# Kernel optimization log

Hardware: AMD Instinct MI355X
Metric: run time of the kernel (lower is better)

The kernel has to match this reference:

```python
import jax, jax.numpy as jnp
import numpy as np

H = 4096       # hidden_size
NH = 32        # num attention heads
DN = 128       # qk_nope_head_dim
DR = 64        # qk_rope_head_dim
DV = 128       # v_head_dim
QL = 1536      # q_lora_rank
KL = 512       # kv_lora_rank
INH = 32       # indexer heads
IHD = 128      # indexer head_dim (== fp8 quant block -> one scale per head)
TOPK = 512     # index_topk
T = 1024       # prefill tokens
SCALING = (DN + DR) ** -0.5
FP8_MAX = 448.0  # e4m3 max


def _rms(x, w, eps=1e-6):
    return x * jax.lax.rsqrt(jnp.mean(x * x, -1, keepdims=True) + eps) * w


def _ln(x, w, b, eps=1e-6):
    m = jnp.mean(x, -1, keepdims=True)
    v = jnp.mean(jnp.square(x - m), -1, keepdims=True)
    return (x - m) * jax.lax.rsqrt(v + eps) * w + b


def _rope(x, pos):
    # interleaved (non-neox) rotary embedding on the last dim
    d = x.shape[-1]
    inv = 1.0 / (10000.0 ** (jnp.arange(0, d, 2, dtype=jnp.float32) / d))
    ang = pos.astype(jnp.float32)[:, None] * inv  # [T, d/2]
    shape = (x.shape[0],) + (1,) * (x.ndim - 2) + (d // 2,)
    cos = jnp.cos(ang).reshape(shape)
    sin = jnp.sin(ang).reshape(shape)
    x1, x2 = x[..., 0::2], x[..., 1::2]
    return jnp.stack([x1 * cos - x2 * sin, x1 * sin + x2 * cos], -1).reshape(x.shape)


def _forward(hidden_states, w_qkv_a, q_a_ln_w, w_q_b, kv_a_ln_w, w_kv_b, w_o,
             w_idx_qb, w_idx_k, idx_k_ln_w, idx_k_ln_b, w_idx_weights, positions):
    Tq = hidden_states.shape[0]
    neg = jnp.finfo(jnp.float32).min
    # --- fused low-rank QKV-a projection ---
    qkv_a = hidden_states @ w_qkv_a                       # [T, QL+KL+DR]
    q_c, kv_c, k_pe = qkv_a[:, :QL], qkv_a[:, QL:QL + KL], qkv_a[:, QL + KL:]
    q_cn = _rms(q_c, q_a_ln_w)                            # qr (normed q latent)
    # --- MLA decompression ---
    q = (q_cn @ w_q_b).reshape(Tq, NH, DN + DR)
    q_nope, q_pe = q[..., :DN], q[..., DN:]
    kv = (_rms(kv_c, kv_a_ln_w) @ w_kv_b).reshape(Tq, NH, DN + DV)
    k_nope, v = kv[..., :DN], kv[..., DN:]
    q_pe = _rope(q_pe, positions)
    k_pe = _rope(k_pe, positions)                         # [T, DR], shared across heads (MQA)
    # --- lightning indexer (fp8 ue8m0 per-token-group quant emulated in fp32) ---
    qi = (q_cn @ w_idx_qb).reshape(Tq, INH, IHD)
    qi = jnp.concatenate([_rope(qi[..., :DR], positions), qi[..., DR:]], -1)
    ki = _ln(hidden_states @ w_idx_k, idx_k_ln_w, idx_k_ln_b)   # [T, IHD]
    ki = jnp.concatenate([_rope(ki[:, :DR], positions), ki[:, DR:]], -1)
    amax = jnp.max(jnp.abs(qi), -1, keepdims=True)        # group == head (IHD == block 128)
    q_scale = jnp.exp2(jnp.ceil(jnp.log2(jnp.maximum(amax, 1e-10) / FP8_MAX)))  # ue8m0
    qi_q = qi / q_scale                                   # values in fp8 range
    wts = (hidden_states @ w_idx_weights) * q_scale[..., 0]
    wts = wts * (IHD ** -0.5) * (INH ** -0.5)             # [T, INH]
    sim = jax.nn.relu(jnp.einsum('qhd,kd->hqk', qi_q, ki))
    logits = jnp.einsum('qh,hqk->qk', wts, sim)           # [Tq, Tk]
    idx = jnp.arange(Tq)
    causal = idx[:, None] >= idx[None, :]
    logits = jnp.where(causal, logits, neg)
    _, topk_idx = jax.lax.top_k(logits, TOPK)             # [T, TOPK]
    sparse_mask = jnp.zeros((Tq, Tq), bool).at[idx[:, None], topk_idx].set(True) & causal
    # --- sparse MLA attention ---
    qf = jnp.concatenate([q_nope, q_pe], -1)              # [T, NH, DN+DR]
    kf = jnp.concatenate([k_nope, jnp.broadcast_to(k_pe[:, None, :], (Tq, NH, DR))], -1)
    scores = jnp.einsum('qhd,khd->hqk', qf, kf) * SCALING
    scores = jnp.where(sparse_mask[None], scores, neg)
    attn = jax.nn.softmax(scores, -1)
    out = jnp.einsum('hqk,khd->qhd', attn, v).reshape(Tq, NH * DV)
    return out @ w_o                                      # [T, H]


def setup_inputs() -> dict:
    key = jax.random.key(0)
    ks = jax.random.split(key, 8)
    s = 0.02
    return {
        'hidden_states': jax.random.normal(ks[0], (T, H), jnp.float32),
        'positions': jnp.arange(T, dtype=jnp.int32),
        'w_qkv_a': jax.random.normal(ks[1], (H, QL + KL + DR), jnp.float32) * s,
        'q_a_ln_w': jnp.ones((QL,), jnp.float32),
        'w_q_b': jax.random.normal(ks[2], (QL, NH * (DN + DR)), jnp.float32) * s,
        'kv_a_ln_w': jnp.ones((KL,), jnp.float32),
        'w_kv_b': jax.random.normal(ks[3], (KL, NH * (DN + DV)), jnp.float32) * s,
        'w_o': jax.random.normal(ks[4], (NH * DV, H), jnp.float32) * s,
        'w_idx_qb': jax.random.normal(ks[5], (QL, INH * IHD), jnp.float32) * s,
        'w_idx_k': jax.random.normal(ks[6], (H, IHD), jnp.float32) * s,
        'idx_k_ln_w': jnp.ones((IHD,), jnp.float32),
        'idx_k_ln_b': jnp.zeros((IHD,), jnp.float32),
        'w_idx_weights': jax.random.normal(ks[7], (H, INH), jnp.float32) * s,
    }


def reference(hidden_states, positions, w_qkv_a, q_a_ln_w, w_q_b, kv_a_ln_w, w_kv_b, w_o,
              w_idx_qb, w_idx_k, idx_k_ln_w, idx_k_ln_b, w_idx_weights):
    return _forward(hidden_states, w_qkv_a, q_a_ln_w, w_q_b, kv_a_ln_w, w_kv_b, w_o,
                    w_idx_qb, w_idx_k, idx_k_ln_w, idx_k_ln_b, w_idx_weights, positions)
```

## Files before the change

kernel.cpp:

```cpp
#include <hip/hip_runtime.h>
#include <hip/hip_bf16.h>
#include <math.h>
#include <type_traits>

#define TT   1024
#define HH   4096
#define NHH  32
#define DNN  128
#define DRR  64
#define DVV  128
#define QLL  1536
#define KLL  512
#define INHH 32
#define IHDD 128
#define TOPKK 512
#define SKS  16
#define SKC  (HH / SKS)
#define QKVN 2112

typedef __attribute__((ext_vector_type(8))) short short8;
typedef __attribute__((ext_vector_type(4))) short short4v;
typedef __attribute__((ext_vector_type(4))) float f32x4;

static __device__ __constant__ float kScaling = 0.07216878364870322f;
static __device__ __constant__ float kWtsScale = 0.015625f;

static __device__ __forceinline__ short f2bf(float f) {
  unsigned u = __float_as_uint(f);
  unsigned r = (u + 0x7fffu + ((u >> 16) & 1u)) >> 16;
  return (short)r;
}
static __device__ __forceinline__ float bf2f(short s) {
  return __uint_as_float(((unsigned)(unsigned short)s) << 16);
}
static __device__ __forceinline__ void gl16(const void* g, void* l) {
  __builtin_amdgcn_global_load_lds(
      (const __attribute__((address_space(1))) unsigned int*)g,
      (__attribute__((address_space(3))) unsigned int*)l, 16, 0, 0);
}
static __device__ __forceinline__ int xcd_swz(int n, int nwg) {
  const int q = nwg >> 3, r = nwg & 7;
  const int x = n & 7, i = n >> 3;
  return (x < r ? x * (q + 1) : r * (q + 1) + (x - r) * q) + i;
}

__global__ __launch_bounds__(256) void skinny_splitk(const float* __restrict__ A,
                                                     const float* __restrict__ B1,
                                                     const float* __restrict__ B2,
                                                     float* __restrict__ part) {
  __shared__ float As[8][64];
  __shared__ float Bs[8][160];
  const int tid = threadIdx.x;
  const int tx = tid & 15, ty = tid >> 4;
  const int bm = blockIdx.x * 64;
  const int kbase = blockIdx.y * SKC;
  float acc[4][10];
#pragma unroll
  for (int i = 0; i < 4; ++i)
#pragma unroll
    for (int j = 0; j < 10; ++j) acc[i][j] = 0.f;
  const int am = tid >> 1, aj = (tid & 1) * 4;
  for (int k0 = 0; k0 < SKC; k0 += 8) {
    __syncthreads();
    if (tid < 128) {
      float4 av = *(const float4*)(A + (size_t)(bm + am) * HH + kbase + k0 + aj);
      As[aj + 0][am] = av.x; As[aj + 1][am] = av.y;
      As[aj + 2][am] = av.z; As[aj + 3][am] = av.w;
    }
#pragma unroll
    for (int i = 0; i < 2; ++i) {
      const int idx = tid + i * 256;
      if (idx < 320) {
        const int row = idx / 40;
        const int c = (idx - row * 40) * 4;
        float4 bv;
        if (c < 128) bv = *(const float4*)(B1 + (size_t)(kbase + k0 + row) * 128 + c);
        else         bv = *(const float4*)(B2 + (size_t)(kbase + k0 + row) * 32 + (c - 128));
        *(float4*)&Bs[row][c] = bv;
      }
    }
    __syncthreads();
#pragma unroll
    for (int p = 0; p < 8; ++p) {
      float av[4];
#pragma unroll
      for (int i = 0; i < 4; ++i) av[i] = As[p][ty * 4 + i];
      float bv[10];
#pragma unroll
      for (int j = 0; j < 10; ++j) bv[j] = Bs[p][tx * 10 + j];
#pragma unroll
      for (int i = 0; i < 4; ++i)
#pragma unroll
        for (int j = 0; j < 10; ++j) acc[i][j] = fmaf(av[i], bv[j], acc[i][j]);
    }
  }
  float* dst = part + ((size_t)blockIdx.y * TT + bm) * 160;
#pragma unroll
  for (int i = 0; i < 4; ++i)
#pragma unroll
    for (int j = 0; j < 10; ++j)
      dst[(size_t)(ty * 4 + i) * 160 + tx * 10 + j] = acc[i][j];
}

__global__ __launch_bounds__(256) void skinny_reduce(const float* __restrict__ part,
                                                     float* __restrict__ kib,
                                                     float* __restrict__ wtsb) {
  const int idx = blockIdx.x * 256 + threadIdx.x;
  const int m = idx / 160, c = idx - m * 160;
  float s = 0.f;
#pragma unroll
  for (int ks = 0; ks < SKS; ++ks) s += part[((size_t)ks * TT + m) * 160 + c];
  if (c < 128) kib[(size_t)m * 128 + c] = s;
  else wtsb[(size_t)m * 32 + (c - 128)] = s;
}

template <typename CT>
__global__ __launch_bounds__(256) void gemm_bf16(const short* __restrict__ A,
                                                 const short* __restrict__ Bt,
                                                 CT* __restrict__ C,
                                                 int M, int N, int K) {
  __shared__ short As[64 * 64];
  __shared__ short Bs[128 * 64];
  int flat = blockIdx.x + gridDim.x * blockIdx.y;
  flat = xcd_swz(flat, gridDim.x * gridDim.y);
  const int byg = flat % gridDim.y;
  const int bxg = flat / gridDim.y;
  const int tid = threadIdx.x;
  const int lane = tid & 63, wv = tid >> 6;
  const int wc = wv * 32;
  const int bm = byg * 64, bn = bxg * 128;
  const int l15 = lane & 15, l4 = lane >> 4;
  const int sx = (l15 & 7) * 8;
  f32x4 acc[4][2];
#pragma unroll
  for (int i = 0; i < 4; ++i)
#pragma unroll
    for (int j = 0; j < 2; ++j) acc[i][j] = f32x4{0.f, 0.f, 0.f, 0.f};
  for (int k0 = 0; k0 < K; k0 += 64) {
    __syncthreads();
#pragma unroll
    for (int i = 0; i < 2; ++i) {
      const int idx = tid + i * 256;
      const int row = idx >> 3, c8 = (idx & 7) * 8;
      const int cs = c8 ^ ((row & 7) * 8);
      gl16(A + (size_t)(bm + row) * K + k0 + cs, &As[idx * 8]);
    }
#pragma unroll
    for (int i = 0; i < 4; ++i) {
      const int idx = tid + i * 256;
      const int row = idx >> 3, c8 = (idx & 7) * 8;
      const int cs = c8 ^ ((row & 7) * 8);
      gl16(Bt + (size_t)(bn + row) * K + k0 + cs, &Bs[idx * 8]);
    }
    __syncthreads();
    short8 fa[4][2], fb[2][2];
#pragma unroll
    for (int rt = 0; rt < 4; ++rt)
#pragma unroll
      for (int kk = 0; kk < 2; ++kk)
        fa[rt][kk] = *(const short8*)(&As[(rt * 16 + l15) * 64 + ((kk * 32 + l4 * 8) ^ sx)]);
#pragma unroll
    for (int ct = 0; ct < 2; ++ct)
#pragma unroll
      for (int kk = 0; kk < 2; ++kk)
        fb[ct][kk] = *(const short8*)(&Bs[(wc + ct * 16 + l15) * 64 + ((kk * 32 + l4 * 8) ^ sx)]);
#pragma unroll
    for (int kk = 0; kk < 2; ++kk)
#pragma unroll
      for (int rt = 0; rt < 4; ++rt)
#pragma unroll
        for (int ct = 0; ct < 2; ++ct)
          acc[rt][ct] = __builtin_amdgcn_mfma_f32_16x16x32_bf16(fa[rt][kk], fb[ct][kk], acc[rt][ct], 0, 0, 0);
  }
#pragma unroll
  for (int rt = 0; rt < 4; ++rt)
#pragma unroll
    for (int ct = 0; ct < 2; ++ct)
#pragma unroll
      for (int r = 0; r < 4; ++r) {
        const int row = bm + rt * 16 + l4 * 4 + r;
        const int col = bn + wc + ct * 16 + l15;
        const float v = acc[rt][ct][r];
        if constexpr (std::is_same<CT, float>::value) C[(size_t)row * N + col] = v;
        else C[(size_t)row * N + col] = __float2bfloat16(v);
      }
}

__global__ __launch_bounds__(256) void gemm1_splitk(const short* __restrict__ A,
                                                    const short* __restrict__ Bt,
                                                    float* __restrict__ part,
                                                    int M, int Np, int K, int kchunk) {
  __shared__ short As[64 * 64];
  __shared__ short Bs[128 * 64];
  int flat = blockIdx.x + gridDim.x * (blockIdx.y + gridDim.y * blockIdx.z);
  flat = xcd_swz(flat, gridDim.x * gridDim.y * gridDim.z);
  const int byg = flat % gridDim.y;
  int tmp = flat / gridDim.y;
  const int bxg = tmp % gridDim.x, bzg = tmp / gridDim.x;
  const int tid = threadIdx.x;
  const int lane = tid & 63, wv = tid >> 6;
  const int wc = wv * 32;
  const int bm = byg * 64, bn = bxg * 128;
  const int kbeg = bzg * kchunk;
  const int l15 = lane & 15, l4 = lane >> 4;
  const int sx = (l15 & 7) * 8;
  f32x4 acc[4][2];
#pragma unroll
  for (int i = 0; i < 4; ++i)
#pragma unroll
    for (int j = 0; j < 2; ++j) acc[i][j] = f32x4{0.f, 0.f, 0.f, 0.f};
  for (int k0 = kbeg; k0 < kbeg + kchunk; k0 += 64) {
    __syncthreads();
#pragma unroll
    for (int i = 0; i < 2; ++i) {
      const int idx = tid + i * 256;
      const int row = idx >> 3, c8 = (idx & 7) * 8;
      const int cs = c8 ^ ((row & 7) * 8);
      gl16(A + (size_t)(bm + row) * K + k0 + cs, &As[idx * 8]);
    }
#pragma unroll
    for (int i = 0; i < 4; ++i) {
      const int idx = tid + i * 256;
      const int row = idx >> 3, c8 = (idx & 7) * 8;
      const int cs = c8 ^ ((row & 7) * 8);
      gl16(Bt + (size_t)(bn + row) * K + k0 + cs, &Bs[idx * 8]);
    }
    __syncthreads();
    short8 fa[4][2], fb[2][2];
#pragma unroll
    for (int rt = 0; rt < 4; ++rt)
#pragma unroll
      for (int kk = 0; kk < 2; ++kk)
        fa[rt][kk] = *(const short8*)(&As[(rt * 16 + l15) * 64 + ((kk * 32 + l4 * 8) ^ sx)]);
#pragma unroll
    for (int ct = 0; ct < 2; ++ct)
#pragma unroll
      for (int kk = 0; kk < 2; ++kk)
        fb[ct][kk] = *(const short8*)(&Bs[(wc + ct * 16 + l15) * 64 + ((kk * 32 + l4 * 8) ^ sx)]);
#pragma unroll
    for (int kk = 0; kk < 2; ++kk)
#pragma unroll
      for (int rt = 0; rt < 4; ++rt)
#pragma unroll
        for (int ct = 0; ct < 2; ++ct)
          acc[rt][ct] = __builtin_amdgcn_mfma_f32_16x16x32_bf16(fa[rt][kk], fb[ct][kk], acc[rt][ct], 0, 0, 0);
  }
  float* dst = part + (size_t)bzg * M * Np;
#pragma unroll
  for (int rt = 0; rt < 4; ++rt)
#pragma unroll
    for (int ct = 0; ct < 2; ++ct)
#pragma unroll
      for (int r = 0; r < 4; ++r)
        dst[(size_t)(bm + rt * 16 + l4 * 4 + r) * Np + bn + wc + ct * 16 + l15] =
            acc[rt][ct][r];
}

__global__ __launch_bounds__(256) void gemm3(const short* __restrict__ Ah,
                                             const short* __restrict__ Al,
                                             const short* __restrict__ Bth,
                                             const short* __restrict__ Btl,
                                             float* __restrict__ part,
                                             int M, int Np, int K, int kchunk) {
  __shared__ short AS[64 * 64], BS[128 * 64];
  int flat = blockIdx.x + gridDim.x * (blockIdx.y + gridDim.y * blockIdx.z);
  flat = xcd_swz(flat, gridDim.x * gridDim.y * gridDim.z);
  const int byg = flat % gridDim.y;
  int tmp = flat / gridDim.y;
  const int bxg = tmp % gridDim.x, bzg = tmp / gridDim.x;
  const int tid = threadIdx.x;
  const int lane = tid & 63, wv = tid >> 6;
  const int wc = wv * 32;
  const int l15 = lane & 15, l4 = lane >> 4;
  const int sx = (l15 & 7) * 8;
  const int bm = byg * 64, bn = bxg * 128;
  const int kbeg = bzg * kchunk;
  f32x4 acc[4][2];
#pragma unroll
  for (int i = 0; i < 4; ++i)
#pragma unroll
    for (int j = 0; j < 2; ++j) acc[i][j] = f32x4{0.f, 0.f, 0.f, 0.f};
  for (int k0 = kbeg; k0 < kbeg + kchunk; k0 += 32) {
    __syncthreads();
#pragma unroll
    for (int i = 0; i < 2; ++i) {
      const int idx = tid + i * 256;
      const int row = idx >> 3, c8 = (idx & 7) * 8;
      const int cs = c8 ^ ((row & 7) * 8);
      const short* srcA = (cs < 32) ? (Ah + (size_t)(bm + row) * K + k0 + cs)
                                    : (Al + (size_t)(bm + row) * K + k0 + (cs - 32));
      gl16(srcA, &AS[idx * 8]);
    }
#pragma unroll
    for (int i = 0; i < 4; ++i) {
      const int idx = tid + i * 256;
      const int row = idx >> 3, c8 = (idx & 7) * 8;
      const int cs = c8 ^ ((row & 7) * 8);
      const short* srcB = (cs < 32) ? (Bth + (size_t)(bn + row) * K + k0 + cs)
                                    : (Btl + (size_t)(bn + row) * K + k0 + (cs - 32));
      gl16(srcB, &BS[idx * 8]);
    }
    __syncthreads();
    short8 fah[4], fal[4], fbh[2], fbl[2];
#pragma unroll
    for (int rt = 0; rt < 4; ++rt) {
      const int row = rt * 16 + l15;
      fah[rt] = *(const short8*)&AS[row * 64 + ((l4 * 8) ^ sx)];
      fal[rt] = *(const short8*)&AS[row * 64 + ((32 + l4 * 8) ^ sx)];
    }
#pragma unroll
    for (int ct = 0; ct < 2; ++ct) {
      const int row = wc + ct * 16 + l15;
      fbh[ct] = *(const short8*)&BS[row * 64 + ((l4 * 8) ^ sx)];
      fbl[ct] = *(const short8*)&BS[row * 64 + ((32 + l4 * 8) ^ sx)];
    }
#pragma unroll
    for (int ct = 0; ct < 2; ++ct)
#pragma unroll
      for (int rt = 0; rt < 4; ++rt) {
        acc[rt][ct] = __builtin_amdgcn_mfma_f32_16x16x32_bf16(fah[rt], fbh[ct], acc[rt][ct], 0, 0, 0);
        acc[rt][ct] = __builtin_amdgcn_mfma_f32_16x16x32_bf16(fah[rt], fbl[ct], acc[rt][ct], 0, 0, 0);
        acc[rt][ct] = __builtin_amdgcn_mfma_f32_16x16x32_bf16(fal[rt], fbh[ct], acc[rt][ct], 0, 0, 0);
      }
  }
  float* dst = part + (size_t)bzg * M * Np;
#pragma unroll
  for (int rt = 0; rt < 4; ++rt)
#pragma unroll
    for (int ct = 0; ct < 2; ++ct)
#pragma unroll
      for (int r = 0; r < 4; ++r)
        dst[(size_t)(bm + rt * 16 + l4 * 4 + r) * Np + bn + wc + ct * 16 + l15] =
            acc[rt][ct][r];
}

__global__ __launch_bounds__(256) void reduce_splitk(const float* __restrict__ part,
                                                     float* __restrict__ C,
                                                     int M, int Np, int Nout, int ldC,
                                                     int ksplit) {
  const int c = blockIdx.x * 256 + threadIdx.x;
  const int m = blockIdx.y;
  if (c >= Nout) return;
  float s = 0.f;
  for (int z = 0; z < ksplit; ++z) s += part[((size_t)z * M + m) * Np + c];
  C[(size_t)m * ldC + c] = s;
}

__global__ __launch_bounds__(256) void qkv_post(const float* __restrict__ qpart,
                                                const float* __restrict__ tpart,
                                                const float* __restrict__ q_ln_w,
                                                const float* __restrict__ kv_ln_w,
                                                const int* __restrict__ pos,
                                                short* __restrict__ qcn_bf,
                                                short* __restrict__ qcn_lo,
                                                short* __restrict__ kvn_bf,
                                                short* __restrict__ kpe_bf) {
  const int t = blockIdx.x, tid = threadIdx.x;
  __shared__ float red[4];
  float qv[6];
  float ss = 0.f;
#pragma unroll
  for (int j = 0; j < 6; ++j) {
    const int c = tid + j * 256;
    float s = 0.f;
#pragma unroll
    for (int z = 0; z < 4; ++z) s += qpart[((size_t)z * TT + t) * QLL + c];
    qv[j] = s;
    ss = fmaf(s, s, ss);
  }
#pragma unroll
  for (int o = 32; o > 0; o >>= 1) ss += __shfl_xor(ss, o);
  if ((tid & 63) == 0) red[tid >> 6] = ss;
  __syncthreads();
  const float rq = rsqrtf((red[0] + red[1] + red[2] + red[3]) / (float)QLL + 1e-6f);
  __syncthreads();
#pragma unroll
  for (int j = 0; j < 6; ++j) {
    const int c = tid + j * 256;
    const float v = qv[j] * rq * q_ln_w[c];
    const short h = f2bf(v);
    qcn_bf[(size_t)t * QLL + c] = h;
    qcn_lo[(size_t)t * QLL + c] = f2bf(v - bf2f(h));
  }
  float kv2[2];
  float ss2 = 0.f;
#pragma unroll
  for (int j = 0; j < 2; ++j) {
    const int c = tid + j * 256;
    float s = 0.f;
#pragma unroll
    for (int z = 0; z < 4; ++z) s += tpart[((size_t)z * TT + t) * 640 + c];
    kv2[j] = s;
    ss2 = fmaf(s, s, ss2);
  }
#pragma unroll
  for (int o = 32; o > 0; o >>= 1) ss2 += __shfl_xor(ss2, o);
  if ((tid & 63) == 0) red[tid >> 6] = ss2;
  __syncthreads();
  const float rkv = rsqrtf((red[0] + red[1] + red[2] + red[3]) / (float)KLL + 1e-6f);
#pragma unroll
  for (int j = 0; j < 2; ++j) {
    const int c = tid + j * 256;
    kvn_bf[(size_t)t * KLL + c] = f2bf(kv2[j] * rkv * kv_ln_w[c]);
  }
  if (tid < 32) {
    float x1 = 0.f, x2 = 0.f;
#pragma unroll
    for (int z = 0; z < 4; ++z) {
      x1 += tpart[((size_t)z * TT + t) * 640 + 512 + 2 * tid];
      x2 += tpart[((size_t)z * TT + t) * 640 + 512 + 2 * tid + 1];
    }
    const float inv = powf(10000.f, -(float)tid * (1.f / 32.f));
    float sn, cs;
    sincosf((float)pos[t] * inv, &sn, &cs);
    kpe_bf[(size_t)t * 64 + 2 * tid]     = f2bf(x1 * cs - x2 * sn);
    kpe_bf[(size_t)t * 64 + 2 * tid + 1] = f2bf(x1 * sn + x2 * cs);
  }
}

__global__ __launch_bounds__(256) void split_cast(const float* __restrict__ in,
                                                  short* __restrict__ hi,
                                                  short* __restrict__ lo, int n4) {
  const int i = blockIdx.x * 256 + threadIdx.x;
  if (i >= n4) return;
  float4 v = *(const float4*)(in + (size_t)i * 4);
  float av[4] = {v.x, v.y, v.z, v.w};
  short4v h, l;
#pragma unroll
  for (int e = 0; e < 4; ++e) {
    h[e] = f2bf(av[e]);
    l[e] = f2bf(av[e] - bf2f(h[e]));
  }
  *(short4v*)(hi + (size_t)i * 4) = h;
  *(short4v*)(lo + (size_t)i * 4) = l;
}

__global__ __launch_bounds__(256) void transpose_cast_g(const float* __restrict__ B,
                                                        short* __restrict__ Bt,
                                                        int K, int ldB, int col0, int Ncols) {
  __shared__ float tile[64][65];
  const int tid = threadIdx.x;
  const int k0 = blockIdx.y * 64, n0 = blockIdx.x * 64;
  const int nl = tid >> 3, kc = (tid & 7) * 8;
  if (n0 >= Ncols) {
    short8 z = {0, 0, 0, 0, 0, 0, 0, 0};
#pragma unroll
    for (int i = 0; i < 2; ++i) {
      const int n = nl + i * 32;
      *(short8*)(Bt + (size_t)(n0 + n) * K + k0 + kc) = z;
    }
    return;
  }
  const int r = tid >> 4, c4 = (tid & 15) * 4;
#pragma unroll
  for (int i = 0; i < 4; ++i) {
    float4 v = *(const float4*)(B + (size_t)(k0 + r + i * 16) * ldB + col0 + n0 + c4);
    tile[r + i * 16][c4 + 0] = v.x;
    tile[r + i * 16][c4 + 1] = v.y;
    tile[r + i * 16][c4 + 2] = v.z;
    tile[r + i * 16][c4 + 3] = v.w;
  }
  __syncthreads();
#pragma unroll
  for (int i = 0; i < 2; ++i) {
    const int n = nl + i * 32;
    short8 o;
#pragma unroll
    for (int e = 0; e < 8; ++e) o[e] = f2bf(tile[kc + e][n]);
    *(short8*)(Bt + (size_t)(n0 + n) * K + k0 + kc) = o;
  }
}

__global__ __launch_bounds__(256) void transpose_split_cast(const float* __restrict__ B,
                                                            short* __restrict__ Bth,
                                                            short* __restrict__ Btl,
                                                            int K, int ldB, int col0,
                                                            int Ncols) {
  __shared__ float tile[64][65];
  const int tid = threadIdx.x;
  const int k0 = blockIdx.y * 64, n0 = blockIdx.x * 64;
  const int nl = tid >> 3, kc = (tid & 7) * 8;
  if (n0 >= Ncols) {
    short8 z = {0, 0, 0, 0, 0, 0, 0, 0};
#pragma unroll
    for (int i = 0; i < 2; ++i) {
      const int n = nl + i * 32;
      *(short8*)(Bth + (size_t)(n0 + n) * K + k0 + kc) = z;
      *(short8*)(Btl + (size_t)(n0 + n) * K + k0 + kc) = z;
    }
    return;
  }
  const int r = tid >> 4, c4 = (tid & 15) * 4;
#pragma unroll
  for (int i = 0; i < 4; ++i) {
    float4 v = *(const float4*)(B + (size_t)(k0 + r + i * 16) * ldB + col0 + n0 + c4);
    tile[r + i * 16][c4 + 0] = v.x;
    tile[r + i * 16][c4 + 1] = v.y;
    tile[r + i * 16][c4 + 2] = v.z;
    tile[r + i * 16][c4 + 3] = v.w;
  }
  __syncthreads();
#pragma unroll
  for (int i = 0; i < 2; ++i) {
    const int n = nl + i * 32;
    short8 oh, ol;
#pragma unroll
    for (int e = 0; e < 8; ++e) {
      const float x = tile[kc + e][n];
      oh[e] = f2bf(x);
      ol[e] = f2bf(x - bf2f(oh[e]));
    }
    *(short8*)(Bth + (size_t)(n0 + n) * K + k0 + kc) = oh;
    *(short8*)(Btl + (size_t)(n0 + n) * K + k0 + kc) = ol;
  }
}

__global__ __launch_bounds__(128) void ki_prep(const float* __restrict__ kin,
                                               const float* __restrict__ w,
                                               const float* __restrict__ b,
                                               const int* __restrict__ pos,
                                               short* __restrict__ kih,
                                               short* __restrict__ kil) {
  const int t = blockIdx.x, i = threadIdx.x;
  float v = kin[(size_t)t * 128 + i];
  float s = v;
#pragma unroll
  for (int o = 32; o > 0; o >>= 1) s += __shfl_xor(s, o);
  __shared__ float r1[2], r2[2];
  if ((i & 63) == 0) r1[i >> 6] = s;
  __syncthreads();
  const float m = (r1[0] + r1[1]) * (1.f / 128.f);
  const float dv = v - m;
  float sq = dv * dv;
#pragma unroll
  for (int o = 32; o > 0; o >>= 1) sq += __shfl_xor(sq, o);
  if ((i & 63) == 0) r2[i >> 6] = sq;
  __syncthreads();
  const float var = (r2[0] + r2[1]) * (1.f / 128.f);
  float x = dv * rsqrtf(var + 1e-6f) * w[i] + b[i];
  if (i < 64) {
    const float part = __shfl_xor(x, 1);
    const int pi = i >> 1;
    const float inv = powf(10000.f, -(float)pi * (1.f / 32.f));
    float sn, cs;
    sincosf((float)pos[t] * inv, &sn, &cs);
    x = (i & 1) ? (part * sn + x * cs) : (x * cs - part * sn);
  }
  const short h = f2bf(x);
  kih[(size_t)t * 128 + i] = h;
  kil[(size_t)t * 128 + i] = f2bf(x - bf2f(h));
}

__global__ void q_rope_repack(const short* __restrict__ qbuf,
                              short* __restrict__ qhout,
                              const int* __restrict__ pos) {
  const int q = blockIdx.x, h = blockIdx.y;
  const int p = threadIdx.x;
  const short* s = qbuf + ((size_t)q * 32 + h) * 192;
  short* d = qhout + ((size_t)h * 1024 + q) * 192;
  float x1 = bf2f(s[2 * p]), x2 = bf2f(s[2 * p + 1]);
  if (p >= 64) {
    const int i = p - 64;
    const float inv = powf(10000.f, -(float)i * (1.f / 32.f));
    const float ang = (float)pos[q] * inv;
    float sn, cs;
    sincosf(ang, &sn, &cs);
    const float a = x1 * cs - x2 * sn, b = x1 * sn + x2 * cs;
    x1 = a; x2 = b;
  }
  d[2 * p]     = f2bf(x1);
  d[2 * p + 1] = f2bf(x2);
}

__global__ __launch_bounds__(256) void qi_rope_repack_split(const float* __restrict__ qib,
                                                            const int* __restrict__ pos,
                                                            short* __restrict__ qhh,
                                                            short* __restrict__ qhl) {
  const int qt = blockIdx.x, h = blockIdx.y;
  const int tid = threadIdx.x;
#pragma unroll
  for (int i = 0; i < 8; ++i) {
    const int idx = tid + i * 256;
    const int q = idx >> 5, c = idx & 31;
    float4 v = *(const float4*)(qib + ((size_t)(qt * 64 + q) * 32 + h) * 128 + c * 4);
    float av[4] = {v.x, v.y, v.z, v.w};
    if (c < 16) {
      const int qg = qt * 64 + q;
      const float p = (float)pos[qg];
      float sn0, cs0, sn1, cs1;
      sincosf(p * powf(10000.f, -(float)(c * 2) * (1.f / 32.f)), &sn0, &cs0);
      sincosf(p * powf(10000.f, -(float)(c * 2 + 1) * (1.f / 32.f)), &sn1, &cs1);
      const float a0 = av[0] * cs0 - av[1] * sn0, a1 = av[0] * sn0 + av[1] * cs0;
      const float a2 = av[2] * cs1 - av[3] * sn1, a3 = av[2] * sn1 + av[3] * cs1;
      av[0] = a0; av[1] = a1; av[2] = a2; av[3] = a3;
    }
    short4v hv, lv;
#pragma unroll
    for (int e = 0; e < 4; ++e) {
      hv[e] = f2bf(av[e]);
      lv[e] = f2bf(av[e] - bf2f(hv[e]));
    }
    const size_t off = ((size_t)h * 1024 + qt * 64 + q) * 128 + c * 4;
    *(short4v*)(qhh + off) = hv;
    *(short4v*)(qhl + off) = lv;
  }
}

__global__ __launch_bounds__(256) void kv_repack(const short* __restrict__ kvb,
                                                 const short* __restrict__ kpe,
                                                 short* __restrict__ kfout,
                                                 short* __restrict__ vtout) {
  const int kt = blockIdx.x, h = blockIdx.y;
  const int tid = threadIdx.x;
  const int k0 = kt * 64;
  __shared__ short vtile[64][136];
#pragma unroll
  for (int i = 0; i < 6; ++i) {
    const int idx = tid + i * 256;
    const int row = idx / 24, c = idx - row * 24;
    short8 v = (c < 16) ? *(const short8*)(kvb + ((size_t)(k0 + row) * 32 + h) * 256 + c * 8)
                        : *(const short8*)(kpe + (size_t)(k0 + row) * 64 + (c - 16) * 8);
    *(short8*)(kfout + ((size_t)h * 1024 + k0 + row) * 192 + c * 8) = v;
  }
#pragma unroll
  for (int i = 0; i < 4; ++i) {
    const int idx = tid + i * 256;
    const int row = idx >> 4, c = idx & 15;
    *(short8*)&vtile[row][c * 8] =
        *(const short8*)(kvb + ((size_t)(k0 + row) * 32 + h) * 256 + 128 + c * 8);
  }
  __syncthreads();
#pragma unroll
  for (int i = 0; i < 4; ++i) {
    const int idx = tid + i * 256;
    const int d = idx >> 3, kc = idx & 7;
    short8 o;
#pragma unroll
    for (int e = 0; e < 8; ++e) o[e] = vtile[kc * 8 + e][d];
    *(short8*)(vtout + ((size_t)h * 128 + d) * 1024 + k0 + kc * 8) = o;
  }
}

__global__ __launch_bounds__(256) void logits_mfma(const short* __restrict__ qih,
                                                   const short* __restrict__ qil,
                                                   const short* __restrict__ kih_g,
                                                   const short* __restrict__ kil_g,
                                                   const float* __restrict__ wts,
                                                   float* __restrict__ part) {
  const int bid = blockIdx.x;
  int bq = (int)((sqrtf(8.f * bid + 1.f) - 1.f) * 0.5f);
  while ((bq + 1) * (bq + 2) / 2 <= bid) ++bq;
  while (bq * (bq + 1) / 2 > bid) --bq;
  const int bk = bid - bq * (bq + 1) / 2;
  const int g = blockIdx.y;
  __shared__ short kih[64 * 128], kil[64 * 128];
  __shared__ float swts[64][16];
  const int tid = threadIdx.x;
  const int lane = tid & 63, wv = tid >> 6;
  const int wr = (wv >> 1) * 32, wc = (wv & 1) * 32;
  const int l15 = lane & 15, l4 = lane >> 4;
  const int q0 = bq * 64, k0 = bk * 64;
  {
    const int r0 = tid >> 4;
    const int c8 = (tid & 15) * 8;
#pragma unroll
    for (int i = 0; i < 4; ++i) {
      const int row = r0 + i * 16;
      gl16(kih_g + (size_t)(k0 + row) * 128 + c8, &kih[(tid + i * 256) * 8]);
      gl16(kil_g + (size_t)(k0 + row) * 128 + c8, &kil[(tid + i * 256) * 8]);
    }
  }
#pragma unroll
  for (int i = 0; i < 4; ++i) {
    const int idx = tid + i * 256;
    swts[idx >> 4][idx & 15] = wts[(size_t)(q0 + (idx >> 4)) * 32 + g * 16 + (idx & 15)];
  }
  __syncthreads();
  short8 kbh[2][4], kbl[2][4];
#pragma unroll
  for (int ct = 0; ct < 2; ++ct)
#pragma unroll
    for (int ks = 0; ks < 4; ++ks) {
      kbh[ct][ks] = *(const short8*)&kih[(wc + ct * 16 + l15) * 128 + ks * 32 + l4 * 8];
      kbl[ct][ks] = *(const short8*)&kil[(wc + ct * 16 + l15) * 128 + ks * 32 + l4 * 8];
    }
  f32x4 lacc[2][2];
#pragma unroll
  for (int i = 0; i < 2; ++i)
#pragma unroll
    for (int j = 0; j < 2; ++j) lacc[i][j] = f32x4{0.f, 0.f, 0.f, 0.f};
  for (int hh = 0; hh < 16; ++hh) {
    const int h = g * 16 + hh;
    short8 qah[2][4], qal[2][4];
#pragma unroll
    for (int rt = 0; rt < 2; ++rt)
#pragma unroll
      for (int ks = 0; ks < 4; ++ks) {
        const size_t off = ((size_t)h * 1024 + q0 + wr + rt * 16 + l15) * 128 + ks * 32 + l4 * 8;
        qah[rt][ks] = *(const short8*)(qih + off);
        qal[rt][ks] = *(const short8*)(qil + off);
      }
    f32x4 hacc[2][2];
#pragma unroll
    for (int i = 0; i < 2; ++i)
#pragma unroll
      for (int j = 0; j < 2; ++j) hacc[i][j] = f32x4{0.f, 0.f, 0.f, 0.f};
#pragma unroll
    for (int ks = 0; ks < 4; ++ks)
#pragma unroll
      for (int rt = 0; rt < 2; ++rt)
#pragma unroll
        for (int ct = 0; ct < 2; ++ct) {
          hacc[rt][ct] = __builtin_amdgcn_mfma_f32_16x16x32_bf16(qah[rt][ks], kbh[ct][ks], hacc[rt][ct], 0, 0, 0);
          hacc[rt][ct] = __builtin_amdgcn_mfma_f32_16x16x32_bf16(qah[rt][ks], kbl[ct][ks], hacc[rt][ct], 0, 0, 0);
          hacc[rt][ct] = __builtin_amdgcn_mfma_f32_16x16x32_bf16(qal[rt][ks], kbh[ct][ks], hacc[rt][ct], 0, 0, 0);
        }
#pragma unroll
    for (int rt = 0; rt < 2; ++rt)
#pragma unroll
      for (int ct = 0; ct < 2; ++ct)
#pragma unroll
        for (int r = 0; r < 4; ++r) {
          const int row = wr + rt * 16 + l4 * 4 + r;
          const float w = swts[row][hh] * kWtsScale;
          lacc[rt][ct][r] = fmaf(w, fmaxf(hacc[rt][ct][r], 0.f), lacc[rt][ct][r]);
        }
  }
#pragma unroll
  for (int rt = 0; rt < 2; ++rt)
#pragma unroll
    for (int ct = 0; ct < 2; ++ct)
#pragma unroll
      for (int r = 0; r < 4; ++r)
        part[(size_t)g * TT * TT + (size_t)(q0 + wr + rt * 16 + l4 * 4 + r) * TT +
             (k0 + wc + ct * 16 + l15)] = lacc[rt][ct][r];
}

__global__ __launch_bounds__(256) void topk_mask(const float* __restrict__ part,
                                                 unsigned* __restrict__ maskbuf) {
  const int w = threadIdx.x >> 6;
  const int lane = threadIdx.x & 63;
  const int q = blockIdx.x * 4 + w;
  const size_t NN = (size_t)TT * TT;
  __shared__ unsigned long long bl[4][16];
  unsigned v[16];
#pragma unroll
  for (int j = 0; j < 16; ++j) {
    const int k = j * 64 + lane;
    unsigned uv = 0u;
    if (k <= q) {
      const size_t o = (size_t)q * TT + k;
      const float s = part[o] + part[NN + o];
      unsigned bb = __float_as_uint(s);
      uv = (bb & 0x80000000u) ? ~bb : (bb | 0x80000000u);
    }
    v[j] = uv;
  }
  if (q + 1 <= TOPKK) {
#pragma unroll
    for (int j = 0; j < 16; ++j) {
      const unsigned long long m = __ballot(j * 64 + lane <= q);
      if (lane == 0) bl[w][j] = m;
    }
  } else {
    unsigned lo = 1u, hi = 0xFFFFFFFFu;
    while (lo < hi) {
      const unsigned mid = lo + ((hi - lo) >> 1) + ((hi - lo) & 1u);
      int c = 0;
#pragma unroll
      for (int j = 0; j < 16; ++j) c += __popcll(__ballot(v[j] >= mid));
      if (c >= TOPKK) lo = mid; else hi = mid - 1u;
    }
    const unsigned ustar = lo;
    int nGreater = 0;
#pragma unroll
    for (int j = 0; j < 16; ++j) nGreater += __popcll(__ballot(v[j] > ustar));
    int need = TOPKK - nGreater;
    const unsigned long long lanemask = lane ? (~0ull >> (64 - lane)) : 0ull;
#pragma unroll
    for (int j = 0; j < 16; ++j) {
      const unsigned long long bg = __ballot(v[j] > ustar);
      const unsigned long long be = __ballot(v[j] == ustar);
      const int ce = __popcll(be);
      const int take = need < ce ? need : ce;
      const int rank = __popcll(be & lanemask);
      const bool selme = ((be >> lane) & 1ull) && (rank < take);
      const unsigned long long m = bg | __ballot(selme);
      if (lane == 0) bl[w][j] = m;
      need -= take;
    }
  }
  __builtin_amdgcn_s_waitcnt(0);
  if (lane < 32)
    maskbuf[(size_t)q * 32 + lane] = (unsigned)(bl[w][lane >> 1] >> ((lane & 1) * 32));
}

__global__ __launch_bounds__(256) void attn_mfma(const short* __restrict__ qh,
                                                 const short* __restrict__ kf,
                                                 const short* __restrict__ vt,
                                                 const unsigned* __restrict__ maskbuf,
                                                 short* __restrict__ ao) {
  const int h = blockIdx.x;
  const int yy = blockIdx.y;
  const int qt = (yy < 8) ? (yy * 2) : (31 - yy * 2);
  const int tid = threadIdx.x;
  const int lane = tid & 63, w = tid >> 6;
  const int l15 = lane & 15, l4 = lane >> 4;
  const int q0 = qt * 64;
  __shared__ short kfs[64 * 200];
  __shared__ short vts[128 * 72];
  __shared__ short ps[4][16][72];
  __shared__ unsigned m32s[64][2];
  short8 qf[6];
#pragma unroll
  for (int ks = 0; ks < 6; ++ks)
    qf[ks] = *(const short8*)(qh + ((size_t)h * 1024 + q0 + w * 16 + l15) * 192 + ks * 32 + l4 * 8);
  f32x4 of[8];
#pragma unroll
  for (int dt = 0; dt < 8; ++dt) of[dt] = f32x4{0.f, 0.f, 0.f, 0.f};
  float m[4], l[4];
#pragma unroll
  for (int r = 0; r < 4; ++r) { m[r] = -INFINITY; l[r] = 0.f; }

  for (int kt = 0; kt <= qt; ++kt) {
    const int k0 = kt * 64;
    __syncthreads();
#pragma unroll
    for (int i = 0; i < 6; ++i) {
      const int idx = tid + i * 256;
      const int row = idx / 24, c = idx - row * 24;
      *(short8*)&kfs[row * 200 + c * 8] =
          *(const short8*)(kf + ((size_t)h * 1024 + k0 + row) * 192 + c * 8);
    }
#pragma unroll
    for (int i = 0; i < 4; ++i) {
      const int idx = tid + i * 256;
      const int row = idx >> 3, c = idx & 7;
      *(short8*)&vts[row * 72 + c * 8] =
          *(const short8*)(vt + ((size_t)h * 128 + row) * 1024 + k0 + c * 8);
    }
    if (tid < 128)
      m32s[tid >> 1][tid & 1] = maskbuf[(size_t)(q0 + (tid >> 1)) * 32 + (k0 >> 5) + (tid & 1)];
    __syncthreads();
    f32x4 sacc[4];
#pragma unroll
    for (int j = 0; j < 4; ++j) sacc[j] = f32x4{0.f, 0.f, 0.f, 0.f};
#pragma unroll
    for (int ks = 0; ks < 6; ++ks)
#pragma unroll
      for (int j = 0; j < 4; ++j) {
        short8 kb = *(const short8*)&kfs[(j * 16 + l15) * 200 + ks * 32 + l4 * 8];
        sacc[j] = __builtin_amdgcn_mfma_f32_16x16x32_bf16(qf[ks], kb, sacc[j], 0, 0, 0);
      }
    float tmax[4] = {-INFINITY, -INFINITY, -INFINITY, -INFINITY};
#pragma unroll
    for (int j = 0; j < 4; ++j)
#pragma unroll
      for (int r = 0; r < 4; ++r) {
        const int kcol = j * 16 + l15;
        const unsigned um = m32s[w * 16 + l4 * 4 + r][kcol >> 5];
        float s = sacc[j][r] * kScaling;
        s = ((um >> (kcol & 31)) & 1u) ? s : -INFINITY;
        sacc[j][r] = s;
        tmax[r] = fmaxf(tmax[r], s);
      }
#pragma unroll
    for (int r = 0; r < 4; ++r) {
      tmax[r] = fmaxf(tmax[r], __shfl_xor(tmax[r], 1));
      tmax[r] = fmaxf(tmax[r], __shfl_xor(tmax[r], 2));
      tmax[r] = fmaxf(tmax[r], __shfl_xor(tmax[r], 4));
      tmax[r] = fmaxf(tmax[r], __shfl_xor(tmax[r], 8));
    }
    float f[4];
#pragma unroll
    for (int r = 0; r < 4; ++r) {
      const float mn = fmaxf(m[r], tmax[r]);
      f[r] = __expf(fmaxf(m[r], -1e30f) - fmaxf(mn, -1e30f));
      m[r] = mn;
      l[r] *= f[r];
    }
    float psum[4] = {0.f, 0.f, 0.f, 0.f};
#pragma unroll
    for (int j = 0; j < 4; ++j)
#pragma unroll
      for (int r = 0; r < 4; ++r) {
        const float p = __expf(sacc[j][r] - fmaxf(m[r], -1e30f));
        psum[r] += p;
        ps[w][l4 * 4 + r][j * 16 + l15] = f2bf(p);
      }
#pragma unroll
    for (int r = 0; r < 4; ++r) {
      psum[r] += __shfl_xor(psum[r], 1);
      psum[r] += __shfl_xor(psum[r], 2);
      psum[r] += __shfl_xor(psum[r], 4);
      psum[r] += __shfl_xor(psum[r], 8);
      l[r] += psum[r];
    }
#pragma unroll
    for (int dt = 0; dt < 8; ++dt)
#pragma unroll
      for (int r = 0; r < 4; ++r) of[dt][r] *= f[r];
    short8 pa0 = *(const short8*)&ps[w][l15][l4 * 8];
    short8 pa1 = *(const short8*)&ps[w][l15][32 + l4 * 8];
#pragma unroll
    for (int dt = 0; dt < 8; ++dt) {
      short8 vb0 = *(const short8*)&vts[(dt * 16 + l15) * 72 + l4 * 8];
      short8 vb1 = *(const short8*)&vts[(dt * 16 + l15) * 72 + 32 + l4 * 8];
      of[dt] = __builtin_amdgcn_mfma_f32_16x16x32_bf16(pa0, vb0, of[dt], 0, 0, 0);
      of[dt] = __builtin_amdgcn_mfma_f32_16x16x32_bf16(pa1, vb1, of[dt], 0, 0, 0);
    }
  }
#pragma unroll
  for (int r = 0; r < 4; ++r) {
    const float invl = 1.f / l[r];
#pragma unroll
    for (int dt = 0; dt < 8; ++dt)
      ao[(size_t)(q0 + w * 16 + l4 * 4 + r) * 4096 + h * 128 + dt * 16 + l15] =
          f2bf(of[dt][r] * invl);
  }
}

extern "C" void kernel_launch(void* const* d_in, const int* in_sizes, int n_in,
                              void* d_out, int out_size, void* d_ws, size_t ws_size,
                              hipStream_t stream) {
  const float* hidden     = (const float*)d_in[0];
  const int*   positions  = (const int*)d_in[1];
  const float* w_qkv_a    = (const float*)d_in[2];
  const float* q_a_ln_w   = (const float*)d_in[3];
  const float* w_q_b      = (const float*)d_in[4];
  const float* kv_a_ln_w  = (const float*)d_in[5];
  const float* w_kv_b     = (const float*)d_in[6];
  const float* w_o        = (const float*)d_in[7];
  const float* w_idx_qb   = (const float*)d_in[8];
  const float* w_idx_k    = (const float*)d_in[9];
  const float* idx_k_ln_w = (const float*)d_in[10];
  const float* idx_k_ln_b = (const float*)d_in[11];
  const float* w_idx_w    = (const float*)d_in[12];
  float* out = (float*)d_out;

  float* ws = (float*)d_ws;
  size_t off = 0;
  auto take = [&](size_t n) { float* p = ws + off; off += n; return p; };
  short* qcn_bf  = (short*)take((size_t)TT * QLL / 2);
  short* qcn_lo  = (short*)take((size_t)TT * QLL / 2);
  short* kvn_bf  = (short*)take((size_t)TT * KLL / 2);
  short* qbuf    = (short*)take((size_t)TT * NHH * 192 / 2);
  short* kvbuf   = (short*)take((size_t)TT * NHH * 256 / 2);
  short* kpe_bf  = (short*)take((size_t)TT * 32);
  float* qib     = take((size_t)TT * INHH * IHDD);
  float* kib     = take((size_t)TT * IHDD);
  float* wtsb    = take((size_t)TT * INHH);
  short* kih_g   = (short*)take((size_t)TT * IHDD / 2);
  short* kil_g   = (short*)take((size_t)TT * IHDD / 2);
  short* qhb     = (short*)take((size_t)NHH * TT * 192 / 2);
  short* qih_h   = (short*)take((size_t)INHH * TT * 128 / 2);
  short* qih_l   = (short*)take((size_t)INHH * TT * 128 / 2);
  short* kfb     = (short*)take((size_t)NHH * TT * 192 / 2);
  short* vtb     = (short*)take((size_t)NHH * 128 * TT / 2);
  float* part4   = take((size_t)4 * TT * TT);
  unsigned* maskbuf = (unsigned*)take((size_t)TT * 32);
  short* hid_h   = (short*)take((size_t)TT * HH / 2);
  short* hid_l   = (short*)take((size_t)TT * HH / 2);
  short* wqkva_h = (short*)take((size_t)QLL * HH / 2);
  short* wqkva_l = (short*)take((size_t)QLL * HH / 2);
  short* wtail_t = (short*)take((size_t)640 * HH / 2);
  short* widxqb_h = (short*)take((size_t)HH * QLL / 2);
  short* widxqb_l = (short*)take((size_t)HH * QLL / 2);
  short* wqb_t   = (short*)take((size_t)6144 * QLL / 2);
  short* wkvb_t  = (short*)take((size_t)8192 * KLL / 2);
  short* ao   = (short*)part4;
  short* wo_t = hid_h;
  float* skpart = part4;
  float* qkvpart = (float*)vtb;
  float* tailpart = (float*)kvbuf;
  float* idxpart = (float*)qhb;

  const dim3 blk(256);
  skinny_splitk<<<dim3(16, SKS), blk, 0, stream>>>(hidden, w_idx_k, w_idx_w, skpart);
  skinny_reduce<<<dim3(TT * 160 / 256), blk, 0, stream>>>(skpart, kib, wtsb);
  split_cast<<<dim3(TT * HH / 4 / 256), blk, 0, stream>>>(hidden, hid_h, hid_l, TT * HH / 4);
  transpose_split_cast<<<dim3(QLL / 64, HH / 64), blk, 0, stream>>>(w_qkv_a, wqkva_h, wqkva_l, HH, QKVN, 0, QLL);
  transpose_cast_g<<<dim3(640 / 64, HH / 64), blk, 0, stream>>>(w_qkv_a, wtail_t, HH, QKVN, QLL, QKVN - QLL);
  transpose_split_cast<<<dim3(HH / 64, QLL / 64), blk, 0, stream>>>(w_idx_qb, widxqb_h, widxqb_l, QLL, HH, 0, HH);
  transpose_cast_g<<<dim3(6144 / 64, QLL / 64), blk, 0, stream>>>(w_q_b, wqb_t, QLL, 6144, 0, 6144);
  transpose_cast_g<<<dim3(8192 / 64, KLL / 64), blk, 0, stream>>>(w_kv_b, wkvb_t, KLL, 8192, 0, 8192);
  ki_prep<<<TT, 128, 0, stream>>>(kib, idx_k_ln_w, idx_k_ln_b, positions, kih_g, kil_g);
  gemm3<<<dim3(QLL / 128, 16, 4), blk, 0, stream>>>(hid_h, hid_l, wqkva_h, wqkva_l,
                                                    qkvpart, TT, QLL, HH, HH / 4);
  gemm1_splitk<<<dim3(5, 16, 4), blk, 0, stream>>>(hid_h, wtail_t, tailpart, TT, 640, HH, HH / 4);
  qkv_post<<<dim3(TT), blk, 0, stream>>>(qkvpart, tailpart, q_a_ln_w, kv_a_ln_w, positions,
                                         qcn_bf, qcn_lo, kvn_bf, kpe_bf);
  transpose_cast_g<<<dim3(HH / 64, HH / 64), blk, 0, stream>>>(w_o, wo_t, HH, HH, 0, HH);
  gemm3<<<dim3(HH / 128, 16, 2), blk, 0, stream>>>(qcn_bf, qcn_lo, widxqb_h, widxqb_l,
                                                   idxpart, TT, HH, QLL, QLL / 2);
  reduce_splitk<<<dim3(HH / 256, TT), blk, 0, stream>>>(idxpart, qib, TT, HH, HH, HH, 2);
  gemm_bf16<__hip_bfloat16><<<dim3(48, 16), blk, 0, stream>>>(qcn_bf, wqb_t, (__hip_bfloat16*)qbuf, TT, 6144, QLL);
  gemm_bf16<__hip_bfloat16><<<dim3(64, 16), blk, 0, stream>>>(kvn_bf, wkvb_t, (__hip_bfloat16*)kvbuf, TT, 8192, KLL);
  q_rope_repack<<<dim3(TT, NHH), 96, 0, stream>>>(qbuf, qhb, positions);
  qi_rope_repack_split<<<dim3(16, INHH), blk, 0, stream>>>(qib, positions, qih_h, qih_l);
  kv_repack<<<dim3(16, NHH), blk, 0, stream>>>(kvbuf, kpe_bf, kfb, vtb);
  logits_mfma<<<dim3(136, 2), blk, 0, stream>>>(qih_h, qih_l, kih_g, kil_g, wtsb, part4);
  topk_mask<<<dim3(TT / 4), blk, 0, stream>>>(part4, maskbuf);
  attn_mfma<<<dim3(NHH, 16), blk, 0, stream>>>(qhb, kfb, vtb, maskbuf, ao);
  gemm_bf16<float><<<dim3(32, 16), blk, 0, stream>>>(ao, wo_t, out, TT, HH, NHH * DVV);
}
```

Baseline: 556.5 us.

## Replace fp32 skinny split-K indexer-key GEMM with split-bf16 MFMA GEMM and fused reduce

The fp32 FMA split-K GEMM that computes the indexer keys and head weights from the hidden states is replaced. The weights are now transposed into hi/lo bf16 pairs padded to 256 columns and fed to the existing three-product MFMA GEMM with split-K 8. The split-K reduction is folded into a new ki_prep2 kernel that also applies the LayerNorm, rope and hi/lo split and writes the head weights, removing two launches. A column guard is added to transpose_split_cast so it can handle the narrow weight matrices, and logits_mfma gets XCD block swizzling. The cost is two extra small transpose launches, padded MFMA work, and more partial-sum traffic.

```diff
diff --git a/kernel.cpp b/kernel.cpp
--- a/kernel.cpp
+++ b/kernel.cpp
@@ -14,8 +14,6 @@
 #define INHH 32
 #define IHDD 128
 #define TOPKK 512
-#define SKS  16
-#define SKC  (HH / SKS)
 #define QKVN 2112
 
 typedef __attribute__((ext_vector_type(8))) short short8;
@@ -42,76 +40,6 @@
   const int q = nwg >> 3, r = nwg & 7;
   const int x = n & 7, i = n >> 3;
   return (x < r ? x * (q + 1) : r * (q + 1) + (x - r) * q) + i;
-}
-
-__global__ __launch_bounds__(256) void skinny_splitk(const float* __restrict__ A,
-                                                     const float* __restrict__ B1,
-                                                     const float* __restrict__ B2,
-                                                     float* __restrict__ part) {
-  __shared__ float As[8][64];
-  __shared__ float Bs[8][160];
-  const int tid = threadIdx.x;
-  const int tx = tid & 15, ty = tid >> 4;
-  const int bm = blockIdx.x * 64;
-  const int kbase = blockIdx.y * SKC;
-  float acc[4][10];
-#pragma unroll
-  for (int i = 0; i < 4; ++i)
-#pragma unroll
-    for (int j = 0; j < 10; ++j) acc[i][j] = 0.f;
-  const int am = tid >> 1, aj = (tid & 1) * 4;
-  for (int k0 = 0; k0 < SKC; k0 += 8) {
-    __syncthreads();
-    if (tid < 128) {
-      float4 av = *(const float4*)(A + (size_t)(bm + am) * HH + kbase + k0 + aj);
-      As[aj + 0][am] = av.x; As[aj + 1][am] = av.y;
-      As[aj + 2][am] = av.z; As[aj + 3][am] = av.w;
-    }
-#pragma unroll
-    for (int i = 0; i < 2; ++i) {
-      const int idx = tid + i * 256;
-      if (idx < 320) {
-        const int row = idx / 40;
-        const int c = (idx - row * 40) * 4;
-        float4 bv;
-        if (c < 128) bv = *(const float4*)(B1 + (size_t)(kbase + k0 + row) * 128 + c);
-        else         bv = *(const float4*)(B2 + (size_t)(kbase + k0 + row) * 32 + (c - 128));
-        *(float4*)&Bs[row][c] = bv;
-      }
-    }
-    __syncthreads();
-#pragma unroll
-    for (int p = 0; p < 8; ++p) {
-      float av[4];
-#pragma unroll
-      for (int i = 0; i < 4; ++i) av[i] = As[p][ty * 4 + i];
-      float bv[10];
-#pragma unroll
-      for (int j = 0; j < 10; ++j) bv[j] = Bs[p][tx * 10 + j];
-#pragma unroll
-      for (int i = 0; i < 4; ++i)
-#pragma unroll
-        for (int j = 0; j < 10; ++j) acc[i][j] = fmaf(av[i], bv[j], acc[i][j]);
-    }
-  }
-  float* dst = part + ((size_t)blockIdx.y * TT + bm) * 160;
-#pragma unroll
-  for (int i = 0; i < 4; ++i)
-#pragma unroll
-    for (int j = 0; j < 10; ++j)
-      dst[(size_t)(ty * 4 + i) * 160 + tx * 10 + j] = acc[i][j];
-}
-
-__global__ __launch_bounds__(256) void skinny_reduce(const float* __restrict__ part,
-                                                     float* __restrict__ kib,
-                                                     float* __restrict__ wtsb) {
-  const int idx = blockIdx.x * 256 + threadIdx.x;
-  const int m = idx / 160, c = idx - m * 160;
-  float s = 0.f;
-#pragma unroll
-  for (int ks = 0; ks < SKS; ++ks) s += part[((size_t)ks * TT + m) * 160 + c];
-  if (c < 128) kib[(size_t)m * 128 + c] = s;
-  else wtsb[(size_t)m * 32 + (c - 128)] = s;
 }
 
 template <typename CT>
@@ -418,6 +346,49 @@
   }
 }
 
+__global__ __launch_bounds__(256) void ki_prep2(const float* __restrict__ part,
+                                                const float* __restrict__ w,
+                                                const float* __restrict__ b,
+                                                const int* __restrict__ pos,
+                                                short* __restrict__ kih,
+                                                short* __restrict__ kil,
+                                                float* __restrict__ wtsb) {
+  const int t = blockIdx.x, tid = threadIdx.x;
+  __shared__ float red[4], red2[4];
+  float s = 0.f;
+#pragma unroll
+  for (int z = 0; z < 8; ++z) s += part[((size_t)z * TT + t) * 256 + tid];
+  if (tid >= 128 && tid < 160) wtsb[(size_t)t * 32 + (tid - 128)] = s;
+  const float v = (tid < 128) ? s : 0.f;
+  float sm = v;
+#pragma unroll
+  for (int o = 32; o > 0; o >>= 1) sm += __shfl_xor(sm, o);
+  if ((tid & 63) == 0) red[tid >> 6] = sm;
+  __syncthreads();
+  const float m = (red[0] + red[1]) * (1.f / 128.f);
+  const float dv = v - m;
+  float sq = (tid < 128) ? dv * dv : 0.f;
+#pragma unroll
+  for (int o = 32; o > 0; o >>= 1) sq += __shfl_xor(sq, o);
+  if ((tid & 63) == 0) red2[tid >> 6] = sq;
+  __syncthreads();
+  const float var = (red2[0] + red2[1]) * (1.f / 128.f);
+  if (tid < 128) {
+    float x = dv * rsqrtf(var + 1e-6f) * w[tid] + b[tid];
+    if (tid < 64) {
+      const float part2 = __shfl_xor(x, 1);
+      const int pi = tid >> 1;
+      const float inv = powf(10000.f, -(float)pi * (1.f / 32.f));
+      float sn, cs;
+      sincosf((float)pos[t] * inv, &sn, &cs);
+      x = (tid & 1) ? (part2 * sn + x * cs) : (x * cs - part2 * sn);
+    }
+    const short h = f2bf(x);
+    kih[(size_t)t * 128 + tid] = h;
+    kil[(size_t)t * 128 + tid] = f2bf(x - bf2f(h));
+  }
+}
+
 __global__ __launch_bounds__(256) void split_cast(const float* __restrict__ in,
                                                   short* __restrict__ hi,
                                                   short* __restrict__ lo, int n4) {
@@ -493,7 +464,9 @@
   const int r = tid >> 4, c4 = (tid & 15) * 4;
 #pragma unroll
   for (int i = 0; i < 4; ++i) {
-    float4 v = *(const float4*)(B + (size_t)(k0 + r + i * 16) * ldB + col0 + n0 + c4);
+    float4 v = make_float4(0.f, 0.f, 0.f, 0.f);
+    if (n0 + c4 < Ncols)
+      v = *(const float4*)(B + (size_t)(k0 + r + i * 16) * ldB + col0 + n0 + c4);
     tile[r + i * 16][c4 + 0] = v.x;
     tile[r + i * 16][c4 + 1] = v.y;
     tile[r + i * 16][c4 + 2] = v.z;
@@ -513,42 +486,6 @@
     *(short8*)(Bth + (size_t)(n0 + n) * K + k0 + kc) = oh;
     *(short8*)(Btl + (size_t)(n0 + n) * K + k0 + kc) = ol;
   }
-}
-
-__global__ __launch_bounds__(128) void ki_prep(const float* __restrict__ kin,
-                                               const float* __restrict__ w,
-                                               const float* __restrict__ b,
-                                               const int* __restrict__ pos,
-                                               short* __restrict__ kih,
-                                               short* __restrict__ kil) {
-  const int t = blockIdx.x, i = threadIdx.x;
-  float v = kin[(size_t)t * 128 + i];
-  float s = v;
-#pragma unroll
-  for (int o = 32; o > 0; o >>= 1) s += __shfl_xor(s, o);
-  __shared__ float r1[2], r2[2];
-  if ((i & 63) == 0) r1[i >> 6] = s;
-  __syncthreads();
-  const float m = (r1[0] + r1[1]) * (1.f / 128.f);
-  const float dv = v - m;
-  float sq = dv * dv;
-#pragma unroll
-  for (int o = 32; o > 0; o >>= 1) sq += __shfl_xor(sq, o);
-  if ((i & 63) == 0) r2[i >> 6] = sq;
-  __syncthreads();
-  const float var = (r2[0] + r2[1]) * (1.f / 128.f);
-  float x = dv * rsqrtf(var + 1e-6f) * w[i] + b[i];
-  if (i < 64) {
-    const float part = __shfl_xor(x, 1);
-    const int pi = i >> 1;
-    const float inv = powf(10000.f, -(float)pi * (1.f / 32.f));
-    float sn, cs;
-    sincosf((float)pos[t] * inv, &sn, &cs);
-    x = (i & 1) ? (part * sn + x * cs) : (x * cs - part * sn);
-  }
-  const short h = f2bf(x);
-  kih[(size_t)t * 128 + i] = h;
-  kil[(size_t)t * 128 + i] = f2bf(x - bf2f(h));
 }
 
 __global__ void q_rope_repack(const short* __restrict__ qbuf,
@@ -647,7 +584,7 @@
                                                    const short* __restrict__ kil_g,
                                                    const float* __restrict__ wts,
                                                    float* __restrict__ part) {
-  const int bid = blockIdx.x;
+  const int bid = xcd_swz(blockIdx.x, gridDim.x);
   int bq = (int)((sqrtf(8.f * bid + 1.f) - 1.f) * 0.5f);
   while ((bq + 1) * (bq + 2) / 2 <= bid) ++bq;
   while (bq * (bq + 1) / 2 > bid) --bq;
@@ -948,7 +885,6 @@
   short* kvbuf   = (short*)take((size_t)TT * NHH * 256 / 2);
   short* kpe_bf  = (short*)take((size_t)TT * 32);
   float* qib     = take((size_t)TT * INHH * IHDD);
-  float* kib     = take((size_t)TT * IHDD);
   float* wtsb    = take((size_t)TT * INHH);
   short* kih_g   = (short*)take((size_t)TT * IHDD / 2);
   short* kil_g   = (short*)take((size_t)TT * IHDD / 2);
@@ -964,6 +900,8 @@
   short* wqkva_h = (short*)take((size_t)QLL * HH / 2);
   short* wqkva_l = (short*)take((size_t)QLL * HH / 2);
   short* wtail_t = (short*)take((size_t)640 * HH / 2);
+  short* wsk_h   = (short*)take((size_t)256 * HH / 2);
+  short* wsk_l   = (short*)take((size_t)256 * HH / 2);
   short* widxqb_h = (short*)take((size_t)HH * QLL / 2);
   short* widxqb_l = (short*)take((size_t)HH * QLL / 2);
   short* wqb_t   = (short*)take((size_t)6144 * QLL / 2);
@@ -976,15 +914,19 @@
   float* idxpart = (float*)qhb;
 
   const dim3 blk(256);
-  skinny_splitk<<<dim3(16, SKS), blk, 0, stream>>>(hidden, w_idx_k, w_idx_w, skpart);
-  skinny_reduce<<<dim3(TT * 160 / 256), blk, 0, stream>>>(skpart, kib, wtsb);
   split_cast<<<dim3(TT * HH / 4 / 256), blk, 0, stream>>>(hidden, hid_h, hid_l, TT * HH / 4);
   transpose_split_cast<<<dim3(QLL / 64, HH / 64), blk, 0, stream>>>(w_qkv_a, wqkva_h, wqkva_l, HH, QKVN, 0, QLL);
   transpose_cast_g<<<dim3(640 / 64, HH / 64), blk, 0, stream>>>(w_qkv_a, wtail_t, HH, QKVN, QLL, QKVN - QLL);
   transpose_split_cast<<<dim3(HH / 64, QLL / 64), blk, 0, stream>>>(w_idx_qb, widxqb_h, widxqb_l, QLL, HH, 0, HH);
+  transpose_split_cast<<<dim3(2, HH / 64), blk, 0, stream>>>(w_idx_k, wsk_h, wsk_l, HH, 128, 0, 128);
+  transpose_split_cast<<<dim3(2, HH / 64), blk, 0, stream>>>(w_idx_w, wsk_h + (size_t)128 * HH,
+                                                            wsk_l + (size_t)128 * HH, HH, 32, 0, 32);
   transpose_cast_g<<<dim3(6144 / 64, QLL / 64), blk, 0, stream>>>(w_q_b, wqb_t, QLL, 6144, 0, 6144);
   transpose_cast_g<<<dim3(8192 / 64, KLL / 64), blk, 0, stream>>>(w_kv_b, wkvb_t, KLL, 8192, 0, 8192);
-  ki_prep<<<TT, 128, 0, stream>>>(kib, idx_k_ln_w, idx_k_ln_b, positions, kih_g, kil_g);
+  gemm3<<<dim3(2, 16, 8), blk, 0, stream>>>(hid_h, hid_l, wsk_h, wsk_l,
+                                            skpart, TT, 256, HH, HH / 8);
+  ki_prep2<<<dim3(TT), blk, 0, stream>>>(skpart, idx_k_ln_w, idx_k_ln_b, positions,
+                                         kih_g, kil_g, wtsb);
   gemm3<<<dim3(QLL / 128, 16, 4), blk, 0, stream>>>(hid_h, hid_l, wqkva_h, wqkva_l,
                                                     qkvpart, TT, QLL, HH, HH / 4);
   gemm1_splitk<<<dim3(5, 16, 4), blk, 0, stream>>>(hid_h, wtail_t, tailpart, TT, 640, HH, HH / 4);
```

After: 518.6 us. 1.07x faster.
